# Performance work log

Hardware: AMD Instinct MI355X
Metric: run time of the kernel (lower is better)

Reference implementation:

```python
import jax, jax.numpy as jnp
import numpy as np
from math import sqrt

HEADS = 16
D_MODEL = 1024
HEAD_DIM = D_MODEL // HEADS  # 64
B, SEQ = 2, 2048


def setup_inputs() -> dict:
    key = jax.random.key(0)
    ks = jax.random.split(key, 8)
    k = jax.random.normal(ks[0], (B, SEQ, D_MODEL), dtype=jnp.float32)
    q = jax.random.normal(ks[1], (B, SEQ, D_MODEL), dtype=jnp.float32)
    v = jax.random.normal(ks[2], (B, SEQ, D_MODEL), dtype=jnp.float32)
    # causal mask, broadcast over batch and heads; masked_fill where mask == 0
    mask = jnp.tril(jnp.ones((SEQ, SEQ), dtype=jnp.int32))[None, None, :, :]
    s = 1.0 / sqrt(HEAD_DIM)
    Wq = jax.random.normal(ks[3], (HEAD_DIM, HEAD_DIM), dtype=jnp.float32) * s
    Wk = jax.random.normal(ks[4], (HEAD_DIM, HEAD_DIM), dtype=jnp.float32) * s
    Wv = jax.random.normal(ks[5], (HEAD_DIM, HEAD_DIM), dtype=jnp.float32) * s
    Wo = jax.random.normal(ks[6], (D_MODEL, D_MODEL), dtype=jnp.float32) * (1.0 / sqrt(D_MODEL))
    bo = jax.random.normal(ks[7], (D_MODEL,), dtype=jnp.float32) * 0.01
    return {"key": k, "query": q, "value": v, "mask": mask,
            "Wq": Wq, "Wk": Wk, "Wv": Wv, "Wo": Wo, "bo": bo}


def reference(key, query, value, mask, Wq, Wk, Wv, Wo, bo):
    b, q_len, d = query.shape
    k_len = key.shape[1]
    hd = d // HEADS
    # reshape to [b, len, heads, head_dim]
    k = key.reshape(b, k_len, HEADS, hd)
    q = query.reshape(b, q_len, HEADS, hd)
    v = value.reshape(b, k_len, HEADS, hd)
    # per-head-dim Linear (weights shared across heads); torch Linear: y = x @ W.T
    k = jnp.einsum('bkhd,ed->bkhe', k, Wk)
    q = jnp.einsum('bqhd,ed->bqhe', q, Wq)
    v = jnp.einsum('bvhd,ed->bvhe', v, Wv)
    # full attention matrix [b, h, q, k]
    product = jnp.einsum('bqhd,bkhd->bhqk', q, k)
    # NOTE: original masks BEFORE scaling by 1/sqrt(head_dim)
    product = jnp.where(mask == 0, jnp.float32(-1e20), product)
    product = product / jnp.float32(sqrt(hd))
    score = jax.nn.softmax(product, axis=-1)
    out = jnp.einsum('bhqv,bvhd->bqhd', score, v).reshape(b, q_len, d)
    out = out @ Wo.T + bo
    return out
```

## Files before the change

### kernel.cpp

```cpp
#include <hip/hip_runtime.h>

typedef __bf16 bf16x8 __attribute__((ext_vector_type(8)));
typedef float  f32x4  __attribute__((ext_vector_type(4)));
typedef float  f32x16 __attribute__((ext_vector_type(16)));
typedef unsigned int uint32x4 __attribute__((ext_vector_type(4)));

#define MFMA16(a, b, c) __builtin_amdgcn_mfma_f32_16x16x32_bf16((a), (b), (c), 0, 0, 0)
#define MFMA32(a, b, c) __builtin_amdgcn_mfma_f32_32x32x16_bf16((a), (b), (c), 0, 0, 0)

#define CVTPK(d, x, y) asm("v_cvt_pk_bf16_f32 %0, %1, %2" : "=v"(d) : "v"(x), "v"(y))
#define PLSWAP(a, b)   asm("v_permlane32_swap_b32 %0, %1" : "+v"(a), "+v"(b))

#define BAR_KEEP_VMEM() asm volatile("s_waitcnt lgkmcnt(0)\n\ts_barrier" ::: "memory")

__device__ inline float fast_exp2(float x) {
#if __has_builtin(__builtin_amdgcn_exp2f)
    return __builtin_amdgcn_exp2f(x);
#else
    return exp2f(x);
#endif
}

constexpr int SEQ = 2048;
constexpr int DM  = 1024;
constexpr int NH  = 16;
constexpr int HD  = 64;
constexpr int BATCH = 2;

__device__ inline bf16x8 ld8_f32(const float* p) {
    f32x4 a = *(const f32x4*)p;
    f32x4 b = *(const f32x4*)(p + 4);
    bf16x8 r;
    r[0] = (__bf16)a[0]; r[1] = (__bf16)a[1]; r[2] = (__bf16)a[2]; r[3] = (__bf16)a[3];
    r[4] = (__bf16)b[0]; r[5] = (__bf16)b[1]; r[6] = (__bf16)b[2]; r[7] = (__bf16)b[3];
    return r;
}

__global__ __launch_bounds__(256)
void proj_kernel(const float* __restrict__ Xq, const float* __restrict__ Xk,
                 const float* __restrict__ Xv,
                 const float* __restrict__ Wq, const float* __restrict__ Wk,
                 const float* __restrict__ Wv,
                 __bf16* __restrict__ Qp, __bf16* __restrict__ Kp,
                 __bf16* __restrict__ Vp)
{
    const int tid  = threadIdx.x;
    const int w    = tid >> 6;
    const int lane = tid & 63;
    const int quad = lane >> 4;
    const int l16  = lane & 15;
    const int sblk = blockIdx.x;
    const int bh   = blockIdx.y;
    const int tz   = blockIdx.z;

    const float* X = (tz == 0) ? Xq : (tz == 1) ? Xk : Xv;
    const float* W = (tz == 0) ? Wq : (tz == 1) ? Wk : Wv;
    __bf16*      O = (tz == 0) ? Qp : (tz == 1) ? Kp : Vp;
    const float scale = (tz == 0) ? (0.125f * 1.44269504088896f) : 1.0f;

    const int b = bh >> 4, h = bh & 15;
    const int mrow = sblk * 64 + w * 16 + l16;

    const size_t xoff = (size_t)(b * SEQ + mrow) * DM + h * HD + quad * 8;
    bf16x8 a0 = ld8_f32(X + xoff);
    bf16x8 a1 = ld8_f32(X + xoff + 32);

    f32x4 acc[4];
    #pragma unroll
    for (int nt = 0; nt < 4; ++nt) {
        const size_t woff = (size_t)(nt * 16 + l16) * HD + quad * 8;
        bf16x8 b0 = ld8_f32(W + woff);
        bf16x8 b1 = ld8_f32(W + woff + 32);
        f32x4 c = {0.f, 0.f, 0.f, 0.f};
        c = MFMA16(a0, b0, c);
        c = MFMA16(a1, b1, c);
        acc[nt] = c;
    }

    __bf16* obase = O + (size_t)bh * SEQ * HD;
    #pragma unroll
    for (int nt = 0; nt < 4; ++nt) {
        #pragma unroll
        for (int r = 0; r < 4; ++r) {
            const int srow = sblk * 64 + w * 16 + quad * 4 + r;
            obase[(size_t)srow * HD + nt * 16 + l16] = (__bf16)(acc[nt][r] * scale);
        }
    }
}

__global__ __launch_bounds__(256, 2)
void attn_kernel(const __bf16* __restrict__ Qp, const __bf16* __restrict__ Kp,
                 const __bf16* __restrict__ Vp, __bf16* __restrict__ AO)
{
    __shared__ __align__(16) unsigned int K_lds[2][64 * 36];
    __shared__ __align__(16) unsigned int VT2[2][64 * 36];

    const int tid  = threadIdx.x;
    const int w    = tid >> 6;
    const int lane = tid & 63;
    const int hi   = lane >> 5;
    const int l32  = lane & 31;
    const int qg   = w >> 1;
    const int kg   = w & 1;

    const int L   = blockIdx.x;
    const int pr  = (L >> 3) & 15;
    const int bh  = (L & 7) + 8 * (L >> 7);

    const __bf16* Qb = Qp + (size_t)bh * SEQ * HD;
    const __bf16* Kb = Kp + (size_t)bh * SEQ * HD;
    const __bf16* Vb = Vp + (size_t)bh * SEQ * HD;

    const int krow = tid >> 3, kcol = tid & 7;
    const int jp = tid & 31, d0 = (tid >> 5) * 8;

    #pragma unroll
    for (int phase = 0; phase < 2; ++phase) {
        const int tile = (phase == 0) ? (31 - pr) : pr;
        const int q0   = tile * 64;
        const int nkc  = tile + 1;

        __syncthreads();

        const __bf16* qp = Qb + (size_t)(q0 + 32 * qg + l32) * HD + hi * 8;
        const bf16x8 qb0 = *(const bf16x8*)(qp);
        const bf16x8 qb1 = *(const bf16x8*)(qp + 16);
        const bf16x8 qb2 = *(const bf16x8*)(qp + 32);
        const bf16x8 qb3 = *(const bf16x8*)(qp + 48);

        f32x16 accO[2];
        #pragma unroll
        for (int et = 0; et < 2; ++et) {
            #pragma unroll
            for (int r = 0; r < 16; ++r) accO[et][r] = 0.f;
        }
        float rs0 = 0.f, rs1 = 0.f;

        uint32x4 kA0, kA1, vAl, vAh, kB0, kB1, vBl, vBh;
        kA0 = *(const uint32x4*)(Kb + (size_t)krow * HD + kcol * 8);
        kA1 = *(const uint32x4*)(Kb + (size_t)(krow + 32) * HD + kcol * 8);
        vAl = *(const uint32x4*)(Vb + (size_t)(2 * jp) * HD + d0);
        vAh = *(const uint32x4*)(Vb + (size_t)(2 * jp + 1) * HD + d0);
        if (nkc > 1) {
            kB0 = *(const uint32x4*)(Kb + (size_t)(64 + krow) * HD + kcol * 8);
            kB1 = *(const uint32x4*)(Kb + (size_t)(64 + krow + 32) * HD + kcol * 8);
            vBl = *(const uint32x4*)(Vb + (size_t)(64 + 2 * jp) * HD + d0);
            vBh = *(const uint32x4*)(Vb + (size_t)(64 + 2 * jp + 1) * HD + d0);
        }

        auto STEP = [&](int kc, int buf, uint32x4& kp0, uint32x4& kp1,
                        uint32x4& vl, uint32x4& vh) {
            *(uint32x4*)&K_lds[buf][krow * 36 + kcol * 4]        = kp0;
            *(uint32x4*)&K_lds[buf][(krow + 32) * 36 + kcol * 4] = kp1;
            #pragma unroll
            for (int i2 = 0; i2 < 4; ++i2) {
                const unsigned int va = vl[i2], vb = vh[i2];
                VT2[buf][(d0 + 2 * i2    ) * 36 + jp] = (va & 0xffffu) | (vb << 16);
                VT2[buf][(d0 + 2 * i2 + 1) * 36 + jp] = (va >> 16) | (vb & 0xffff0000u);
            }

            if (kc + 2 < nkc) {
                const size_t o = (size_t)(kc + 2) * 64;
                kp0 = *(const uint32x4*)(Kb + (o + krow) * HD + kcol * 8);
                kp1 = *(const uint32x4*)(Kb + (o + krow + 32) * HD + kcol * 8);
                vl  = *(const uint32x4*)(Vb + (o + 2 * jp) * HD + d0);
                vh  = *(const uint32x4*)(Vb + (o + 2 * jp + 1) * HD + d0);
            }
            BAR_KEEP_VMEM();

            if (!(kc == tile && qg == 0 && kg == 1)) {
                const __bf16* kp = (const __bf16*)&K_lds[buf][(32 * kg + l32) * 36] + hi * 8;
                f32x16 s;
                #pragma unroll
                for (int r = 0; r < 16; ++r) s[r] = 0.f;
                __builtin_amdgcn_s_setprio(1);
                s = MFMA32(*(const bf16x8*)(kp),      qb0, s);
                s = MFMA32(*(const bf16x8*)(kp + 16), qb1, s);
                s = MFMA32(*(const bf16x8*)(kp + 32), qb2, s);
                s = MFMA32(*(const bf16x8*)(kp + 48), qb3, s);
                __builtin_amdgcn_s_setprio(0);

                if (kc == tile && qg == kg) {
                    #pragma unroll
                    for (int r = 0; r < 16; ++r) {
                        const int cr = (r & 3) + 8 * (r >> 2) + 4 * hi;
                        if (cr > l32) s[r] = -1e30f;
                    }
                }

                float p[16];
                #pragma unroll
                for (int r = 0; r < 16; ++r) p[r] = fast_exp2(s[r]);
                #pragma unroll
                for (int r = 0; r < 8; ++r) { rs0 += p[2 * r]; rs1 += p[2 * r + 1]; }

                unsigned int w0, w1, w2, w3, w4, w5, w6, w7;
                CVTPK(w0, p[0],  p[1]);  CVTPK(w1, p[2],  p[3]);
                CVTPK(w2, p[4],  p[5]);  CVTPK(w3, p[6],  p[7]);
                CVTPK(w4, p[8],  p[9]);  CVTPK(w5, p[10], p[11]);
                CVTPK(w6, p[12], p[13]); CVTPK(w7, p[14], p[15]);
                PLSWAP(w0, w2); PLSWAP(w1, w3); PLSWAP(w4, w6); PLSWAP(w5, w7);
                uint32x4 u0 = {w0, w1, w2, w3};
                uint32x4 u1 = {w4, w5, w6, w7};
                const bf16x8 pa0 = *(const bf16x8*)&u0;
                const bf16x8 pa1 = *(const bf16x8*)&u1;

                __builtin_amdgcn_s_setprio(1);
                #pragma unroll
                for (int et = 0; et < 2; ++et) {
                    const __bf16* vp = (const __bf16*)&VT2[buf][(et * 32 + l32) * 36]
                                       + 32 * kg + hi * 8;
                    accO[et] = MFMA32(pa0, *(const bf16x8*)(vp),      accO[et]);
                    accO[et] = MFMA32(pa1, *(const bf16x8*)(vp + 16), accO[et]);
                }
                __builtin_amdgcn_s_setprio(0);
            }
        };

        for (int kc = 0; kc < nkc; kc += 2) {
            STEP(kc, 0, kA0, kA1, vAl, vAh);
            if (kc + 1 < nkc) STEP(kc + 1, 1, kB0, kB1, vBl, vBh);
        }

        __syncthreads();
        float* red = (float*)K_lds;
        float rsum = rs0 + rs1;
        if (kg == 1) {
            float* dst = red + (size_t)(qg * 64 + lane) * 33;
            #pragma unroll
            for (int r = 0; r < 16; ++r) { dst[r] = accO[0][r]; dst[16 + r] = accO[1][r]; }
            dst[32] = rsum;
        }
        __syncthreads();
        if (kg == 0) {
            const float* src = red + (size_t)(qg * 64 + lane) * 33;
            #pragma unroll
            for (int r = 0; r < 16; ++r) { accO[0][r] += src[r]; accO[1][r] += src[16 + r]; }
            rsum += src[32];
            const float rt  = rsum + __shfl_xor(rsum, 32, 64);
            const float ivq = 1.0f / rt;
            const int b = bh >> 4, h = bh & 15;
            #pragma unroll
            for (int r = 0; r < 16; ++r) {
                const int cr = (r & 3) + 8 * (r >> 2) + 4 * hi;
                const float iv = __shfl(ivq, cr, 64);
                __bf16* ao = AO + (size_t)(b * SEQ + q0 + 32 * qg + cr) * DM + h * HD;
                ao[l32]      = (__bf16)(accO[0][r] * iv);
                ao[32 + l32] = (__bf16)(accO[1][r] * iv);
            }
        }
    }
}

__global__ __launch_bounds__(256)
void wconv_kernel(const float* __restrict__ Wo, __bf16* __restrict__ Wb)
{
    const size_t i = ((size_t)blockIdx.x * 256 + threadIdx.x) * 8;
    *(bf16x8*)(Wb + i) = ld8_f32(Wo + i);
}

__global__ __launch_bounds__(256)
void ogemm_kernel(const __bf16* __restrict__ AO, const __bf16* __restrict__ Wb,
                  const float* __restrict__ bo, float* __restrict__ out)
{
    __shared__ __align__(16) unsigned int A_lds[2][64 * 36];
    __shared__ __align__(16) unsigned int B_lds[2][64 * 36];

    const int tid  = threadIdx.x;
    const int w    = tid >> 6;
    const int lane = tid & 63;
    const int hi   = lane >> 5;
    const int l32  = lane & 31;
    const int wm   = w >> 1;
    const int wn   = w & 1;

    const int L   = blockIdx.x;
    const int xcd = L & 7;
    const int r_  = L >> 3;
    const int n0  = (r_ & 15) * 64;
    const int m0  = (xcd * 8 + (r_ >> 4)) * 64;

    const int row = tid >> 3, c = tid & 7;

    f32x16 acc;
    #pragma unroll
    for (int r = 0; r < 16; ++r) acc[r] = 0.f;

    uint32x4 aA[2], bA[2], aB[2], bB[2];
    #pragma unroll
    for (int i = 0; i < 2; ++i) {
        aA[i] = *(const uint32x4*)(AO + (size_t)(m0 + row + i * 32) * DM + c * 8);
        bA[i] = *(const uint32x4*)(Wb + (size_t)(n0 + row + i * 32) * DM + c * 8);
        aB[i] = *(const uint32x4*)(AO + (size_t)(m0 + row + i * 32) * DM + 64 + c * 8);
        bB[i] = *(const uint32x4*)(Wb + (size_t)(n0 + row + i * 32) * DM + 64 + c * 8);
    }

    auto GSTEP = [&](int kc, int buf, uint32x4 (&ap)[2], uint32x4 (&bp)[2]) {
        #pragma unroll
        for (int i = 0; i < 2; ++i) {
            *(uint32x4*)&A_lds[buf][(row + i * 32) * 36 + c * 4] = ap[i];
            *(uint32x4*)&B_lds[buf][(row + i * 32) * 36 + c * 4] = bp[i];
        }

        if (kc + 2 < DM / 64) {
            const size_t o = (size_t)(kc + 2) * 64;
            #pragma unroll
            for (int i = 0; i < 2; ++i) {
                ap[i] = *(const uint32x4*)(AO + (size_t)(m0 + row + i * 32) * DM + o + c * 8);
                bp[i] = *(const uint32x4*)(Wb + (size_t)(n0 + row + i * 32) * DM + o + c * 8);
            }
        }
        BAR_KEEP_VMEM();

        const __bf16* ap2 = (const __bf16*)&A_lds[buf][(wm * 32 + l32) * 36] + hi * 8;
        const __bf16* bp2 = (const __bf16*)&B_lds[buf][(wn * 32 + l32) * 36] + hi * 8;
        #pragma unroll
        for (int f = 0; f < 4; ++f)
            acc = MFMA32(*(const bf16x8*)(ap2 + 16 * f),
                         *(const bf16x8*)(bp2 + 16 * f), acc);
    };

    for (int kc = 0; kc < DM / 64; kc += 2) {
        GSTEP(kc,     0, aA, bA);
        GSTEP(kc + 1, 1, aB, bB);
    }

    const int n = n0 + wn * 32 + l32;
    const float bof = bo[n];
    #pragma unroll
    for (int r = 0; r < 16; ++r) {
        const int cr = (r & 3) + 8 * (r >> 2) + 4 * hi;
        out[(size_t)(m0 + wm * 32 + cr) * DM + n] = acc[r] + bof;
    }
}

extern "C" void kernel_launch(void* const* d_in, const int* in_sizes, int n_in,
                              void* d_out, int out_size, void* d_ws, size_t ws_size,
                              hipStream_t stream)
{
    const float* key   = (const float*)d_in[0];
    const float* query = (const float*)d_in[1];
    const float* value = (const float*)d_in[2];
    const float* Wq = (const float*)d_in[4];
    const float* Wk = (const float*)d_in[5];
    const float* Wv = (const float*)d_in[6];
    const float* Wo = (const float*)d_in[7];
    const float* bo = (const float*)d_in[8];

    const size_t per = (size_t)BATCH * NH * SEQ * HD;
    __bf16* Qp = (__bf16*)d_ws;
    __bf16* Kp = Qp + per;
    __bf16* Vp = Kp + per;
    __bf16* AO = Vp + per;
    __bf16* Wb = Kp;

    proj_kernel<<<dim3(SEQ / 64, BATCH * NH, 3), 256, 0, stream>>>(
        query, key, value, Wq, Wk, Wv, Qp, Kp, Vp);
    attn_kernel<<<dim3(16 * BATCH * NH), 256, 0, stream>>>(Qp, Kp, Vp, AO);
    wconv_kernel<<<dim3(DM * DM / (256 * 8)), 256, 0, stream>>>(Wo, Wb);
    ogemm_kernel<<<dim3(64 * 16), 256, 0, stream>>>(
        AO, Wb, bo, (float*)d_out);
}
```

Measured before the change: 183.8 us.

## Load K fragments directly from global into MFMA registers, bypassing LDS

```diff
diff --git a/kernel.cpp b/kernel.cpp
--- a/kernel.cpp
+++ b/kernel.cpp
@@ -92,7 +92,6 @@
 void attn_kernel(const __bf16* __restrict__ Qp, const __bf16* __restrict__ Kp,
                  const __bf16* __restrict__ Vp, __bf16* __restrict__ AO)
 {
-    __shared__ __align__(16) unsigned int K_lds[2][64 * 36];
     __shared__ __align__(16) unsigned int VT2[2][64 * 36];
 
     const int tid  = threadIdx.x;
@@ -111,8 +110,9 @@
     const __bf16* Kb = Kp + (size_t)bh * SEQ * HD;
     const __bf16* Vb = Vp + (size_t)bh * SEQ * HD;
 
-    const int krow = tid >> 3, kcol = tid & 7;
     const int jp = tid & 31, d0 = (tid >> 5) * 8;
+
+    const __bf16* Kfrag = Kb + (size_t)(32 * kg + l32) * HD + hi * 8;
 
     #pragma unroll
     for (int phase = 0; phase < 2; ++phase) {
@@ -136,49 +136,57 @@
         }
         float rs0 = 0.f, rs1 = 0.f;
 
-        uint32x4 kA0, kA1, vAl, vAh, kB0, kB1, vBl, vBh;
-        kA0 = *(const uint32x4*)(Kb + (size_t)krow * HD + kcol * 8);
-        kA1 = *(const uint32x4*)(Kb + (size_t)(krow + 32) * HD + kcol * 8);
+        bf16x8 kA0, kA1, kA2, kA3, kB0, kB1, kB2, kB3;
+        uint32x4 vAl, vAh, vBl, vBh;
+        kA0 = *(const bf16x8*)(Kfrag);
+        kA1 = *(const bf16x8*)(Kfrag + 16);
+        kA2 = *(const bf16x8*)(Kfrag + 32);
+        kA3 = *(const bf16x8*)(Kfrag + 48);
         vAl = *(const uint32x4*)(Vb + (size_t)(2 * jp) * HD + d0);
         vAh = *(const uint32x4*)(Vb + (size_t)(2 * jp + 1) * HD + d0);
         if (nkc > 1) {
-            kB0 = *(const uint32x4*)(Kb + (size_t)(64 + krow) * HD + kcol * 8);
-            kB1 = *(const uint32x4*)(Kb + (size_t)(64 + krow + 32) * HD + kcol * 8);
+            const __bf16* kf1 = Kfrag + (size_t)64 * HD;
+            kB0 = *(const bf16x8*)(kf1);
+            kB1 = *(const bf16x8*)(kf1 + 16);
+            kB2 = *(const bf16x8*)(kf1 + 32);
+            kB3 = *(const bf16x8*)(kf1 + 48);
             vBl = *(const uint32x4*)(Vb + (size_t)(64 + 2 * jp) * HD + d0);
             vBh = *(const uint32x4*)(Vb + (size_t)(64 + 2 * jp + 1) * HD + d0);
         }
 
-        auto STEP = [&](int kc, int buf, uint32x4& kp0, uint32x4& kp1,
-                        uint32x4& vl, uint32x4& vh) {
-            *(uint32x4*)&K_lds[buf][krow * 36 + kcol * 4]        = kp0;
-            *(uint32x4*)&K_lds[buf][(krow + 32) * 36 + kcol * 4] = kp1;
+        auto STEP = [&](int kc, int buf, bf16x8& k0, bf16x8& k1, bf16x8& k2,
+                        bf16x8& k3, uint32x4& vl, uint32x4& vh) {
             #pragma unroll
             for (int i2 = 0; i2 < 4; ++i2) {
                 const unsigned int va = vl[i2], vb = vh[i2];
                 VT2[buf][(d0 + 2 * i2    ) * 36 + jp] = (va & 0xffffu) | (vb << 16);
                 VT2[buf][(d0 + 2 * i2 + 1) * 36 + jp] = (va >> 16) | (vb & 0xffff0000u);
             }
-
             if (kc + 2 < nkc) {
                 const size_t o = (size_t)(kc + 2) * 64;
-                kp0 = *(const uint32x4*)(Kb + (o + krow) * HD + kcol * 8);
-                kp1 = *(const uint32x4*)(Kb + (o + krow + 32) * HD + kcol * 8);
-                vl  = *(const uint32x4*)(Vb + (o + 2 * jp) * HD + d0);
-                vh  = *(const uint32x4*)(Vb + (o + 2 * jp + 1) * HD + d0);
+                vl = *(const uint32x4*)(Vb + (o + 2 * jp) * HD + d0);
+                vh = *(const uint32x4*)(Vb + (o + 2 * jp + 1) * HD + d0);
             }
             BAR_KEEP_VMEM();
 
             if (!(kc == tile && qg == 0 && kg == 1)) {
-                const __bf16* kp = (const __bf16*)&K_lds[buf][(32 * kg + l32) * 36] + hi * 8;
                 f32x16 s;
                 #pragma unroll
                 for (int r = 0; r < 16; ++r) s[r] = 0.f;
                 __builtin_amdgcn_s_setprio(1);
-                s = MFMA32(*(const bf16x8*)(kp),      qb0, s);
-                s = MFMA32(*(const bf16x8*)(kp + 16), qb1, s);
-                s = MFMA32(*(const bf16x8*)(kp + 32), qb2, s);
-                s = MFMA32(*(const bf16x8*)(kp + 48), qb3, s);
+                s = MFMA32(k0, qb0, s);
+                s = MFMA32(k1, qb1, s);
+                s = MFMA32(k2, qb2, s);
+                s = MFMA32(k3, qb3, s);
                 __builtin_amdgcn_s_setprio(0);
+
+                if (kc + 2 < nkc) {
+                    const __bf16* kf = Kfrag + (size_t)(kc + 2) * 64 * HD;
+                    k0 = *(const bf16x8*)(kf);
+                    k1 = *(const bf16x8*)(kf + 16);
+                    k2 = *(const bf16x8*)(kf + 32);
+                    k3 = *(const bf16x8*)(kf + 48);
+                }
 
                 if (kc == tile && qg == kg) {
                     #pragma unroll
@@ -218,12 +226,12 @@
         };
 
         for (int kc = 0; kc < nkc; kc += 2) {
-            STEP(kc, 0, kA0, kA1, vAl, vAh);
-            if (kc + 1 < nkc) STEP(kc + 1, 1, kB0, kB1, vBl, vBh);
+            STEP(kc, 0, kA0, kA1, kA2, kA3, vAl, vAh);
+            if (kc + 1 < nkc) STEP(kc + 1, 1, kB0, kB1, kB2, kB3, vBl, vBh);
         }
 
         __syncthreads();
-        float* red = (float*)K_lds;
+        float* red = (float*)VT2;
         float rsum = rs0 + rs1;
         if (kg == 1) {
             float* dst = red + (size_t)(qg * 64 + lane) * 33;
```

Result: slower. 199.7 us (+8.6%).
